# Optimization experiments

Measured on AMD Instinct MI355X. Metric: run time of the kernel, lower is better.

Reference implementation:

```python
import jax, jax.numpy as jnp
import numpy as np

TEMPERATURE = 1.0
B, D = 8192, 256


def setup_inputs() -> dict:
    key = jax.random.key(0)
    k1, k2 = jax.random.split(key)
    return {
        "encoder_embedding1": jax.random.normal(k1, (B, D), dtype=jnp.float32),
        "encoder_embedding2": jax.random.normal(k2, (B, D), dtype=jnp.float32),
    }


def _l2_normalize(x, eps=1e-8):
    # matches torch CosineSimilarity eps handling closely enough for fp32
    n = jnp.sqrt(jnp.sum(x * x, axis=-1, keepdims=True))
    return x / jnp.maximum(n, eps)


def reference(encoder_embedding1, encoder_embedding2):
    # sim[i, j] = cos(contrast_i, anchor_j); torch builds this via a (B,B,D)
    # expand + elementwise CosineSimilarity — here it's a normalized matmul.
    a = _l2_normalize(encoder_embedding1)  # anchors  [B, D]
    c = _l2_normalize(encoder_embedding2)  # contrast [B, D]
    sim = jnp.einsum("id,jd->ij", c, a)    # [B, B]
    log_probs = jax.nn.log_softmax(sim / TEMPERATURE, axis=0)
    loss = -jnp.sum(jnp.diagonal(log_probs)) * TEMPERATURE
    return loss
```

## Files before the change

### kernel.cpp

```cpp
#include <hip/hip_runtime.h>
#include <hip/hip_bf16.h>
#include <hip/hip_fp8.h>


#define BROWS 8192
#define DIM   256

typedef float f32x4 __attribute__((ext_vector_type(4)));

__device__ __forceinline__ void gload_lds16(const void* g, void* l) {
  __builtin_amdgcn_global_load_lds(
      (const __attribute__((address_space(1))) unsigned int*)g,
      (__attribute__((address_space(3))) unsigned int*)l, 16, 0, 0);
}

__device__ __forceinline__ unsigned char to_e4m3(float v) {
  __hip_fp8_e4m3 t(v);
  return *reinterpret_cast<unsigned char*>(&t);
}

__global__ __launch_bounds__(256) void prep_kernel(
    const float* __restrict__ E1, const float* __restrict__ E2,
    unsigned char* __restrict__ An8, unsigned char* __restrict__ Cn8,
    float* __restrict__ diag, float* __restrict__ colsum) {
  if (blockIdx.x < 32) colsum[blockIdx.x * 256 + threadIdx.x] = 0.f;

  const int w    = threadIdx.x >> 6;
  const int lane = threadIdx.x & 63;
  const int row  = blockIdx.x * 4 + w;
  const size_t base = (size_t)row * DIM + lane * 4;

  const float4 a = *(const float4*)(E1 + base);
  const float4 c = *(const float4*)(E2 + base);

  float sa  = a.x*a.x + a.y*a.y + a.z*a.z + a.w*a.w;
  float sc  = c.x*c.x + c.y*c.y + c.z*c.z + c.w*c.w;
  float sac = a.x*c.x + a.y*c.y + a.z*c.z + a.w*c.w;
#pragma unroll
  for (int o = 32; o > 0; o >>= 1) {
    sa  += __shfl_down(sa,  o);
    sc  += __shfl_down(sc,  o);
    sac += __shfl_down(sac, o);
  }
  const float inva = 1.0f / fmaxf(sqrtf(__shfl(sa, 0)), 1e-8f);
  const float invc = 1.0f / fmaxf(sqrtf(__shfl(sc, 0)), 1e-8f);

  uchar4 pa, pc;
  pa.x = to_e4m3(a.x * inva); pa.y = to_e4m3(a.y * inva);
  pa.z = to_e4m3(a.z * inva); pa.w = to_e4m3(a.w * inva);
  pc.x = to_e4m3(c.x * invc); pc.y = to_e4m3(c.y * invc);
  pc.z = to_e4m3(c.z * invc); pc.w = to_e4m3(c.w * invc);
  *(uchar4*)(An8 + base) = pa;
  *(uchar4*)(Cn8 + base) = pc;
  if (lane == 0) diag[row] = sac * inva * invc;
}

__global__ __launch_bounds__(256, 4) void gemm_colsum_kernel(
    const unsigned char* __restrict__ Cn8,
    const unsigned char* __restrict__ An8,
    float* __restrict__ colsum) {
  __shared__ __align__(16) char ldsC[2][8192];
  __shared__ __align__(16) char ldsA[2][8192];
  __shared__ float ldscol[2][128];

  const int tid  = threadIdx.x;
  const int lane = tid & 63;
  const int w    = tid >> 6;
  const int wr   = w >> 1;
  const int wc   = w & 1;

  const int jtile = blockIdx.x & 63;
  const int itile = blockIdx.x >> 6;
  const int i0 = itile * 128;
  const int j0 = jtile * 128;

  const int srow = w * 32 + (lane >> 2);
  const int sblk = (lane & 3) ^ ((lane >> 3) & 3);
  const unsigned char* gC = Cn8 + (size_t)(i0 + srow) * DIM + sblk * 16;
  const unsigned char* gA = An8 + (size_t)(j0 + srow) * DIM + sblk * 16;
  char* lbC0 = &ldsC[0][0] + w * 2048;
  char* lbA0 = &ldsA[0][0] + w * 2048;

  auto stage = [&](int ks, int buf) {
    const int gk = ks * 64;
    char* lc = lbC0 + buf * 8192;
    char* la = lbA0 + buf * 8192;
#pragma unroll
    for (int j = 0; j < 2; ++j) {
      gload_lds16(gC + (size_t)j * 16 * DIM + gk, lc + j * 1024);
      gload_lds16(gA + (size_t)j * 16 * DIM + gk, la + j * 1024);
    }
  };

  f32x4 acc[4][4] = {};

  stage(0, 0);
  stage(1, 1);

  const int q     = lane >> 4;
  const int rsw   = ((lane & 15) >> 1) & 3;
  const int rbase = lane & 15;

#pragma unroll
  for (int t = 0; t < 4; ++t) {
    const int b = t & 1;
    if (t < 3) { asm volatile("s_waitcnt vmcnt(4)" ::: "memory"); }
    else       { asm volatile("s_waitcnt vmcnt(0)" ::: "memory"); }
    __builtin_amdgcn_sched_barrier(0);
    __builtin_amdgcn_s_barrier();

    long long af[2][4], bfv[2][4];
#pragma unroll
    for (int kk = 0; kk < 2; ++kk) {
      const int c    = kk * 4 + q;
      const int boff = (((c >> 1) ^ rsw) << 4) + ((c & 1) << 3);
#pragma unroll
      for (int m = 0; m < 4; ++m) {
        const int r = wr * 64 + m * 16 + rbase;
        af[kk][m] = *(const long long*)(&ldsC[b][0] + r * 64 + boff);
      }
#pragma unroll
      for (int n = 0; n < 4; ++n) {
        const int r = wc * 64 + n * 16 + rbase;
        bfv[kk][n] = *(const long long*)(&ldsA[b][0] + r * 64 + boff);
      }
    }
    asm volatile("s_waitcnt lgkmcnt(0)" ::: "memory");
    __builtin_amdgcn_sched_barrier(0);
    __builtin_amdgcn_s_barrier();
    __builtin_amdgcn_sched_barrier(0);

    if (t < 2) stage(t + 2, b);
    __builtin_amdgcn_sched_barrier(0);

    __builtin_amdgcn_s_setprio(1);
#pragma unroll
    for (int kk = 0; kk < 2; ++kk)
#pragma unroll
      for (int m = 0; m < 4; ++m)
#pragma unroll
        for (int n = 0; n < 4; ++n)
          acc[m][n] = __builtin_amdgcn_mfma_f32_16x16x32_fp8_fp8(
              af[kk][m], bfv[kk][n], acc[m][n], 0, 0, 0);
    __builtin_amdgcn_s_setprio(0);
  }

#pragma unroll
  for (int n = 0; n < 4; ++n) {
    float s = 0.f;
#pragma unroll
    for (int m = 0; m < 4; ++m) {
      const f32x4 v = acc[m][n];
      s += __expf(v[0]) + __expf(v[1]) + __expf(v[2]) + __expf(v[3]);
    }
    s += __shfl_xor(s, 16);
    s += __shfl_xor(s, 32);
    if (lane < 16) ldscol[wr][wc * 64 + n * 16 + lane] = s;
  }
  __syncthreads();
  if (tid < 128) {
    const float v = ldscol[0][tid] + ldscol[1][tid];
    atomicAdd(&colsum[j0 + tid], v);
  }
}

__global__ __launch_bounds__(256) void finalize_kernel(
    const float* __restrict__ colsum, const float* __restrict__ diag,
    float* __restrict__ out) {
  const int t = threadIdx.x;
  float s = 0.f;
  for (int j = t; j < BROWS; j += 256) s += logf(colsum[j]) - diag[j];
#pragma unroll
  for (int o = 32; o > 0; o >>= 1) s += __shfl_down(s, o);
  __shared__ float red[4];
  if ((t & 63) == 0) red[t >> 6] = s;
  __syncthreads();
  if (t == 0) out[0] = red[0] + red[1] + red[2] + red[3];
}

extern "C" void kernel_launch(void* const* d_in, const int* in_sizes, int n_in,
                              void* d_out, int out_size, void* d_ws, size_t ws_size,
                              hipStream_t stream) {
  const float* E1 = (const float*)d_in[0];
  const float* E2 = (const float*)d_in[1];
  char* ws = (char*)d_ws;
  unsigned char* Cn8 = (unsigned char*)(ws);
  unsigned char* An8 = (unsigned char*)(ws + (size_t)2 * 1024 * 1024);
  float* colsum = (float*)(ws + (size_t)4 * 1024 * 1024);
  float* diag   = (float*)(ws + (size_t)4 * 1024 * 1024 + 32 * 1024);
  float* out = (float*)d_out;

  prep_kernel<<<BROWS / 4, 256, 0, stream>>>(E1, E2, An8, Cn8, diag, colsum);
  gemm_colsum_kernel<<<(BROWS / 128) * (BROWS / 128), 256, 0, stream>>>(Cn8, An8, colsum);
  finalize_kernel<<<1, 256, 0, stream>>>(colsum, diag, out);
}
```

Before: 48.94 us.

## Use scaled 16x16x128 FP8 MFMA with full-K LDS staging

Replaces the double-buffered 64-wide K pipeline with a single load of the full 256-wide K slice of both tiles into LDS, using a new XOR swizzle. The inner product now uses the gfx950 scaled MFMA 16x16x128 f8f6f4 instruction with unit scales (0x7F), which cuts the MFMA count by four and reads 32-byte fragments. LDS per block grows to 64KB and the occupancy hint drops to two blocks per CU. The cost is that global loads no longer overlap with compute inside a block.

After: 50.88 us. +4.0%, slower.

```diff
diff --git a/kernel.cpp b/kernel.cpp
--- a/kernel.cpp
+++ b/kernel.cpp
@@ -6,6 +6,8 @@
 #define BROWS 8192
 #define DIM   256
 
+typedef int   i32x4 __attribute__((ext_vector_type(4)));
+typedef int   i32x8 __attribute__((ext_vector_type(8)));
 typedef float f32x4 __attribute__((ext_vector_type(4)));
 
 __device__ __forceinline__ void gload_lds16(const void* g, void* l) {
@@ -55,12 +57,12 @@
   if (lane == 0) diag[row] = sac * inva * invc;
 }
 
-__global__ __launch_bounds__(256, 4) void gemm_colsum_kernel(
+__global__ __launch_bounds__(256, 2) void gemm_colsum_kernel(
     const unsigned char* __restrict__ Cn8,
     const unsigned char* __restrict__ An8,
     float* __restrict__ colsum) {
-  __shared__ __align__(16) char ldsC[2][8192];
-  __shared__ __align__(16) char ldsA[2][8192];
+  __shared__ __align__(16) unsigned char ldsC[128 * 256];
+  __shared__ __align__(16) unsigned char ldsA[128 * 256];
   __shared__ float ldscol[2][128];
 
   const int tid  = threadIdx.x;
@@ -74,74 +76,56 @@
   const int i0 = itile * 128;
   const int j0 = jtile * 128;
 
-  const int srow = w * 32 + (lane >> 2);
-  const int sblk = (lane & 3) ^ ((lane >> 3) & 3);
-  const unsigned char* gC = Cn8 + (size_t)(i0 + srow) * DIM + sblk * 16;
-  const unsigned char* gA = An8 + (size_t)(j0 + srow) * DIM + sblk * 16;
-  char* lbC0 = &ldsC[0][0] + w * 2048;
-  char* lbA0 = &ldsA[0][0] + w * 2048;
+  const int sr = tid >> 4;
+  const int pl = (tid & 15) ^ (sr & 7);
+  const unsigned char* gC = Cn8 + (size_t)(i0 + sr) * DIM + pl * 16;
+  const unsigned char* gA = An8 + (size_t)(j0 + sr) * DIM + pl * 16;
 
-  auto stage = [&](int ks, int buf) {
-    const int gk = ks * 64;
-    char* lc = lbC0 + buf * 8192;
-    char* la = lbA0 + buf * 8192;
 #pragma unroll
-    for (int j = 0; j < 2; ++j) {
-      gload_lds16(gC + (size_t)j * 16 * DIM + gk, lc + j * 1024);
-      gload_lds16(gA + (size_t)j * 16 * DIM + gk, la + j * 1024);
-    }
-  };
+  for (int j = 0; j < 8; ++j) {
+    gload_lds16(gC + (size_t)j * 16 * DIM, &ldsC[0] + j * 4096 + w * 1024);
+    gload_lds16(gA + (size_t)j * 16 * DIM, &ldsA[0] + j * 4096 + w * 1024);
+  }
+  asm volatile("s_waitcnt vmcnt(0)" ::: "memory");
+  __builtin_amdgcn_sched_barrier(0);
+  __builtin_amdgcn_s_barrier();
 
   f32x4 acc[4][4] = {};
-
-  stage(0, 0);
-  stage(1, 1);
-
-  const int q     = lane >> 4;
-  const int rsw   = ((lane & 15) >> 1) & 3;
-  const int rbase = lane & 15;
+  const int q  = lane >> 4;
+  const int rb = lane & 15;
+  const int SC = 0x7F7F7F7F;
 
 #pragma unroll
-  for (int t = 0; t < 4; ++t) {
-    const int b = t & 1;
-    if (t < 3) { asm volatile("s_waitcnt vmcnt(4)" ::: "memory"); }
-    else       { asm volatile("s_waitcnt vmcnt(0)" ::: "memory"); }
-    __builtin_amdgcn_sched_barrier(0);
-    __builtin_amdgcn_s_barrier();
-
-    long long af[2][4], bfv[2][4];
+  for (int W = 0; W < 2; ++W) {
+    i32x8 af[4], bfv[4];
 #pragma unroll
-    for (int kk = 0; kk < 2; ++kk) {
-      const int c    = kk * 4 + q;
-      const int boff = (((c >> 1) ^ rsw) << 4) + ((c & 1) << 3);
+    for (int m = 0; m < 4; ++m) {
+      const int r  = wr * 64 + m * 16 + rb;
+      const int s0 = (W * 8 + q * 2)     ^ (r & 7);
+      const int s1 = (W * 8 + q * 2 + 1) ^ (r & 7);
+      union { i32x4 h[2]; i32x8 v; } u;
+      u.h[0] = *(const i32x4*)(&ldsC[0] + r * 256 + s0 * 16);
+      u.h[1] = *(const i32x4*)(&ldsC[0] + r * 256 + s1 * 16);
+      af[m] = u.v;
+    }
 #pragma unroll
-      for (int m = 0; m < 4; ++m) {
-        const int r = wr * 64 + m * 16 + rbase;
-        af[kk][m] = *(const long long*)(&ldsC[b][0] + r * 64 + boff);
-      }
-#pragma unroll
-      for (int n = 0; n < 4; ++n) {
-        const int r = wc * 64 + n * 16 + rbase;
-        bfv[kk][n] = *(const long long*)(&ldsA[b][0] + r * 64 + boff);
-      }
+    for (int n = 0; n < 4; ++n) {
+      const int r  = wc * 64 + n * 16 + rb;
+      const int s0 = (W * 8 + q * 2)     ^ (r & 7);
+      const int s1 = (W * 8 + q * 2 + 1) ^ (r & 7);
+      union { i32x4 h[2]; i32x8 v; } u;
+      u.h[0] = *(const i32x4*)(&ldsA[0] + r * 256 + s0 * 16);
+      u.h[1] = *(const i32x4*)(&ldsA[0] + r * 256 + s1 * 16);
+      bfv[n] = u.v;
     }
-    asm volatile("s_waitcnt lgkmcnt(0)" ::: "memory");
-    __builtin_amdgcn_sched_barrier(0);
-    __builtin_amdgcn_s_barrier();
-    __builtin_amdgcn_sched_barrier(0);
-
-    if (t < 2) stage(t + 2, b);
-    __builtin_amdgcn_sched_barrier(0);
-
     __builtin_amdgcn_s_setprio(1);
 #pragma unroll
-    for (int kk = 0; kk < 2; ++kk)
+    for (int m = 0; m < 4; ++m)
 #pragma unroll
-      for (int m = 0; m < 4; ++m)
-#pragma unroll
-        for (int n = 0; n < 4; ++n)
-          acc[m][n] = __builtin_amdgcn_mfma_f32_16x16x32_fp8_fp8(
-              af[kk][m], bfv[kk][n], acc[m][n], 0, 0, 0);
+      for (int n = 0; n < 4; ++n)
+        acc[m][n] = __builtin_amdgcn_mfma_scale_f32_16x16x128_f8f6f4(
+            af[m], bfv[n], acc[m][n], 0 , 0 ,
+            0, SC, 0, SC);
     __builtin_amdgcn_s_setprio(0);
   }
 
```
